# Kernel tuning notes

Measured on AMD Instinct MI355X. Metric: run time of the kernel, lower is better.

The kernel has to match this reference:

```python
import jax, jax.numpy as jnp
import numpy as np

KAPPA = 80.0
NORM_EPS = 0.1
NORM_MAX = 14.0
VOCAB, EMBED, HIDDEN = 50257, 512, 1024
B, S = 2048, 128


def _sample_w(key, kappa, dim, batch):
    """Batched vMF rejection sampler for the radial weight w (Wood 1994).
    Vectorizes the per-row python while-loop of the original module."""
    dim_r = dim - 1
    b = dim_r / (np.sqrt(4.0 * kappa ** 2 + dim_r ** 2) + 2.0 * kappa)
    x = (1.0 - b) / (1.0 + b)
    c = kappa * x + dim_r * np.log(1.0 - x ** 2)
    b = np.float32(b); x = np.float32(x); c = np.float32(c)
    kap = np.float32(kappa); dr = np.float32(dim_r)

    def cond(st):
        return ~jnp.all(st[2])

    def body(st):
        key, w, acc = st
        key, k1, k2 = jax.random.split(key, 3)
        z = jax.random.beta(k1, dim_r / 2.0, dim_r / 2.0, (batch,), dtype=jnp.float32)
        wn = (1.0 - (1.0 + b) * z) / (1.0 - (1.0 - b) * z)
        u = jax.random.uniform(k2, (batch,), dtype=jnp.float32)
        ok = (kap * wn + dr * jnp.log(1.0 - x * wn) - c) >= jnp.log(u)
        w = jnp.where(ok & ~acc, wn, w)
        return key, w, acc | ok

    init = (key, jnp.zeros((batch,), jnp.float32), jnp.zeros((batch,), bool))
    _, w, _ = jax.lax.while_loop(cond, body, init)
    return w


def _vmf_sample(mu, key):
    B_, D = mu.shape
    kw, kv, kt, kf1, kf2 = jax.random.split(key, 5)
    w = _sample_w(kw, KAPPA, D, B_)                       # [B]
    v_raw = jax.random.normal(kv, (B_, D), jnp.float32)
    trand = jax.random.uniform(kt, (B_,), jnp.float32) * NORM_EPS

    munorm = jnp.linalg.norm(mu, axis=1)                  # [B]
    munoise = jnp.clip(munorm, 0.0, NORM_MAX - NORM_EPS) + trand
    safe = jnp.maximum(munorm, 1e-20)
    mu_hat = mu / safe[:, None]
    # sample direction orthonormal to mu_hat
    proj = jnp.sum(mu_hat * v_raw, axis=1, keepdims=True)
    ortho = v_raw - mu_hat * proj
    v = ortho / jnp.linalg.norm(ortho, axis=1, keepdims=True)
    w_ = w[:, None]
    main = (v * jnp.sqrt(1.0 - w_ ** 2) + mu_hat * w_) * munoise[:, None]
    # degenerate branch (||mu|| ~ 0): random small vector
    rd = jax.random.normal(kf1, (B_, D), jnp.float32)
    rd = rd / jnp.linalg.norm(rd, axis=1, keepdims=True)
    fb = rd * (jax.random.uniform(kf2, (B_, 1), jnp.float32) * NORM_EPS)
    return jnp.where((munorm > 1e-10)[:, None], main, fb)


def setup_inputs() -> dict:
    key = jax.random.key(0)
    k1, k2, k3, k4 = jax.random.split(key, 4)
    return {
        "added_tokens": jax.random.randint(k1, (B, S), 0, VOCAB, dtype=jnp.int32).astype(jnp.int64),
        "removed_tokens": jax.random.randint(k2, (B, S), 0, VOCAB, dtype=jnp.int32).astype(jnp.int64),
        "embed_table": jax.random.normal(k3, (VOCAB, EMBED), jnp.float32) * 0.02,
        "w_prenoise": jax.random.normal(k4, (HIDDEN // 2, EMBED), jnp.float32) * 0.02,
    }


def reference(added_tokens, removed_tokens, embed_table, w_prenoise):
    emb_add_sum = embed_table[added_tokens].sum(1)        # [B, EMBED]
    emb_rem_sum = embed_table[removed_tokens].sum(1)      # [B, EMBED]
    insert_set = emb_add_sum @ w_prenoise.T               # [B, HIDDEN/2]
    delete_set = emb_rem_sum @ w_prenoise.T               # [B, HIDDEN/2]
    combined = jnp.concatenate([insert_set, delete_set], axis=1)  # [B, HIDDEN]
    return _vmf_sample(combined, jax.random.key(42))
```

## Files before the change

kernel.cpp:

```cpp
#include <hip/hip_runtime.h>
#include <hip/hip_fp16.h>
#include <stdint.h>
#include <math.h>

#define NROWS 2048
#define SEQ   128
#define EMB   512
#define HID   1024
#define VOCAB 50257
#define GR    4
#define NSPEC 8

typedef _Float16 f16x4 __attribute__((ext_vector_type(4)));
typedef float    f32x4 __attribute__((ext_vector_type(4)));

struct U2 { uint32_t x, y; };

__device__ __forceinline__ uint32_t rotl32(uint32_t v, int r) {
  return (v << r) | (v >> (32 - r));
}

__device__ __forceinline__ U2 tf2x32(U2 key, uint32_t x0, uint32_t x1) {
  uint32_t ks0 = key.x, ks1 = key.y;
  uint32_t ks2 = ks0 ^ ks1 ^ 0x1BD11BDAu;
  x0 += ks0; x1 += ks1;
  x0 += x1; x1 = rotl32(x1, 13); x1 ^= x0;
  x0 += x1; x1 = rotl32(x1, 15); x1 ^= x0;
  x0 += x1; x1 = rotl32(x1, 26); x1 ^= x0;
  x0 += x1; x1 = rotl32(x1, 6);  x1 ^= x0;
  x0 += ks1; x1 += ks2 + 1u;
  x0 += x1; x1 = rotl32(x1, 17); x1 ^= x0;
  x0 += x1; x1 = rotl32(x1, 29); x1 ^= x0;
  x0 += x1; x1 = rotl32(x1, 16); x1 ^= x0;
  x0 += x1; x1 = rotl32(x1, 24); x1 ^= x0;
  x0 += ks2; x1 += ks0 + 2u;
  x0 += x1; x1 = rotl32(x1, 13); x1 ^= x0;
  x0 += x1; x1 = rotl32(x1, 15); x1 ^= x0;
  x0 += x1; x1 = rotl32(x1, 26); x1 ^= x0;
  x0 += x1; x1 = rotl32(x1, 6);  x1 ^= x0;
  x0 += ks0; x1 += ks1 + 3u;
  x0 += x1; x1 = rotl32(x1, 17); x1 ^= x0;
  x0 += x1; x1 = rotl32(x1, 29); x1 ^= x0;
  x0 += x1; x1 = rotl32(x1, 16); x1 ^= x0;
  x0 += x1; x1 = rotl32(x1, 24); x1 ^= x0;
  x0 += ks1; x1 += ks2 + 4u;
  x0 += x1; x1 = rotl32(x1, 13); x1 ^= x0;
  x0 += x1; x1 = rotl32(x1, 15); x1 ^= x0;
  x0 += x1; x1 = rotl32(x1, 26); x1 ^= x0;
  x0 += x1; x1 = rotl32(x1, 6);  x1 ^= x0;
  x0 += ks2; x1 += ks0 + 5u;
  U2 r; r.x = x0; r.y = x1; return r;
}

__device__ __forceinline__ U2 tf_subkey(U2 key, uint32_t i) { return tf2x32(key, 0u, i); }
__device__ __forceinline__ uint32_t tf_bits32(U2 key, uint32_t idx) {
  U2 r = tf2x32(key, 0u, idx);
  return r.x ^ r.y;
}

__device__ __forceinline__ float unit_from_bits(uint32_t b) {
  uint32_t fb = (b >> 9) | 0x3f800000u;
  return __uint_as_float(fb) - 1.0f;
}

__device__ __forceinline__ float f32_log(float x)  { return (float)log((double)x); }
__device__ __forceinline__ float f32_exp(float x)  { return (float)exp((double)x); }
__device__ __forceinline__ float f32_log1p(float x){ return (float)log1p((double)x); }

__device__ float erfinv32(float x) {
#pragma clang fp contract(off)
  float nxx = -(x * x);
  float w = -f32_log1p(nxx);
  float p;
  if (w < 5.0f) {
    w = w - 2.5f;
    p = 2.81022636e-08f;
    p = 3.43273939e-07f  + p * w;
    p = -3.5233877e-06f  + p * w;
    p = -4.39150654e-06f + p * w;
    p = 0.00021858087f   + p * w;
    p = -0.00125372503f  + p * w;
    p = -0.00417768164f  + p * w;
    p = 0.246640727f     + p * w;
    p = 1.50140941f      + p * w;
  } else {
    w = sqrtf(w) - 3.0f;
    p = -0.000200214257f;
    p = 0.000100950558f  + p * w;
    p = 0.00134934322f   + p * w;
    p = -0.00367342844f  + p * w;
    p = 0.00573950773f   + p * w;
    p = -0.0076224613f   + p * w;
    p = 0.00943887047f   + p * w;
    p = 1.00167406f      + p * w;
    p = 2.83297682f      + p * w;
  }
  return p * x;
}

__device__ __forceinline__ float normal_from_bits(uint32_t bits) {
#pragma clang fp contract(off)
  float u = unit_from_bits(bits);
  const float LO = -0.99999994f;
  float x = u * 2.0f + LO;
  x = fmaxf(LO, x);
  return 1.4142135623730951f * erfinv32(x);
}

__device__ float loggamma_511_5(U2 gkey) {
#pragma clang fp contract(off)
  const float one_third = 1.0f / 3.0f;
  const float d = 511.5f - one_third;
  const float c = one_third / sqrtf(d);
  U2 key = tf_subkey(gkey, 0u);
  float V = 1.0f;
  for (int it = 0; it < 64; ++it) {
    U2 knext = tf_subkey(key, 0u);
    U2 xkey  = tf_subkey(key, 1u);
    U2 Ukey  = tf_subkey(key, 2u);
    float x, v;
    U2 xk = xkey;
    do {
      U2 xk_next = tf_subkey(xk, 0u);
      U2 nsub    = tf_subkey(xk, 1u);
      x = normal_from_bits(tf_bits32(nsub, 0u));
      v = 1.0f + x * c;
      xk = xk_next;
    } while (v <= 0.0f);
    float X = x * x;
    V = (v * v) * v;
    float U = unit_from_bits(tf_bits32(Ukey, 0u));
    float sq = 1.0f - 0.0331f * (X * X);
    bool cont;
    if (!(U >= sq)) {
      cont = false;
    } else {
      float logU = f32_log(U);
      float thr = X * 0.5f + d * ((1.0f - V) + f32_log(V));
      cont = (logU >= thr);
    }
    if (!cont) break;
    key = knext;
  }
  return f32_log(d) + f32_log(V);
}

__device__ float beta_elem(U2 k1, uint32_t i) {
#pragma clang fp contract(off)
  U2 ka = tf_subkey(k1, 0u);
  U2 kb = tf_subkey(k1, 1u);
  U2 ga = tf_subkey(ka, i);
  U2 gb = tf_subkey(kb, i);
  float lga = loggamma_511_5(ga);
  float lgb = loggamma_511_5(gb);
  float m  = fmaxf(lga, lgb);
  float ea = f32_exp(lga - m);
  float eb = f32_exp(lgb - m);
  return ea / (ea + eb);
}

__device__ __forceinline__ bool wood_try(U2 K, uint32_t i, float& wn) {
#pragma clang fp contract(off)
  const double kappa_d = 80.0, dimr_d = 1023.0;
  const double b_d = dimr_d / (sqrt(4.0 * kappa_d * kappa_d + dimr_d * dimr_d) + 2.0 * kappa_d);
  const double x_d = (1.0 - b_d) / (1.0 + b_d);
  const double c_d = kappa_d * x_d + dimr_d * log(1.0 - x_d * x_d);
  const float bf = (float)b_d, xf = (float)x_d, cf = (float)c_d;
  const float b1p = 1.0f + bf, b1m = 1.0f - bf;

  U2 k1 = tf_subkey(K, 1u);
  U2 k2 = tf_subkey(K, 2u);
  float z = beta_elem(k1, i);
  wn = (1.0f - b1p * z) / (1.0f - b1m * z);
  float u = unit_from_bits(tf_bits32(k2, i));
  float lhs = (80.0f * wn + 1023.0f * f32_log(1.0f - xf * wn)) - cf;
  return lhs >= f32_log(u);
}

__device__ float wood_seq_from(U2 K, uint32_t i, int t_start) {
  float w = 0.0f;
  for (int t = t_start; t < 64; ++t) {
    U2 Kn = tf_subkey(K, 0u);
    float wn;
    if (wood_try(K, i, wn)) { w = wn; break; }
    K = Kn;
  }
  return w;
}

#define NWOODBLK 64
#define NBLK_W   128
#define NBLK_E   ((VOCAB + 3) / 4)

__device__ __forceinline__ uint2 cvt4h(float4 a) {
  union { __half h[4]; uint2 u; } pk;
  pk.h[0] = __float2half(a.x); pk.h[1] = __float2half(a.y);
  pk.h[2] = __float2half(a.z); pk.h[3] = __float2half(a.w);
  return pk.u;
}

__device__ __forceinline__ uint32_t quant4(float4 a, float inv) {
  int q0 = __float2int_rn(a.x * inv);
  int q1 = __float2int_rn(a.y * inv);
  int q2 = __float2int_rn(a.z * inv);
  int q3 = __float2int_rn(a.w * inv);
  q0 = max(-127, min(127, q0)); q1 = max(-127, min(127, q1));
  q2 = max(-127, min(127, q2)); q3 = max(-127, min(127, q3));
  return (uint32_t)(uint8_t)q0 | ((uint32_t)(uint8_t)q1 << 8) |
         ((uint32_t)(uint8_t)q2 << 16) | ((uint32_t)(uint8_t)q3 << 24);
}

__global__ __launch_bounds__(256) void convert_kernel(
    const float* __restrict__ embed, const float* __restrict__ W,
    int8_t* __restrict__ embed_i8, float* __restrict__ scales,
    __half* __restrict__ W_h,
    float* __restrict__ spec_w, uint32_t* __restrict__ spec_ok) {
  int b = blockIdx.x;
  int wave = threadIdx.x >> 6, lane = threadIdx.x & 63;
  if (b < NWOODBLK) {
    int g = b * 256 + threadIdx.x;
    int t = g >> 11;
    int i = g & (NROWS - 1);
    U2 key42; key42.x = 0u; key42.y = 42u;
    U2 K = tf_subkey(key42, 0u);
    for (int j = 0; j < t; ++j) K = tf_subkey(K, 0u);
    float wn;
    bool ok = wood_try(K, (uint32_t)i, wn);
    spec_w[t * NROWS + i]  = wn;
    spec_ok[t * NROWS + i] = ok ? 1u : 0u;
  } else if (b < NWOODBLK + NBLK_W) {
    int wid = (b - NWOODBLK) * 4 + wave;
    size_t base = (size_t)wid * 128 + lane;
    const float4* src = (const float4*)W;
    uint2* dst = (uint2*)W_h;
    float4 a = src[base];
    float4 c = src[base + 64];
    dst[base]      = cvt4h(a);
    dst[base + 64] = cvt4h(c);
  } else {
    int wid = (b - NWOODBLK - NBLK_W) * 4 + wave;
    if (wid < VOCAB) {
      size_t base = (size_t)wid * 128 + lane;
      const float4* src = (const float4*)embed;
      float4 a = src[base];
      float4 c = src[base + 64];
      float m = fmaxf(fmaxf(fmaxf(fabsf(a.x), fabsf(a.y)), fmaxf(fabsf(a.z), fabsf(a.w))),
                      fmaxf(fmaxf(fabsf(c.x), fabsf(c.y)), fmaxf(fabsf(c.z), fabsf(c.w))));
#pragma unroll
      for (int off = 1; off < 64; off <<= 1) m = fmaxf(m, __shfl_xor(m, off, 64));
      float inv   = (m > 0.0f) ? 127.0f / m : 0.0f;
      float scale = (m > 0.0f) ? m / 127.0f : 0.0f;
      uint32_t* dst = (uint32_t*)embed_i8;
      size_t b32 = (size_t)wid * 128 + lane;
      dst[b32]      = quant4(a, inv);
      dst[b32 + 64] = quant4(c, inv);
      if (lane == 0) scales[wid] = scale;
    }
  }
}

__global__ __launch_bounds__(256) void gather_sum_i8_kernel(
    const int* __restrict__ add_tok, const int* __restrict__ rem_tok,
    const int8_t* __restrict__ embed_i8, const float* __restrict__ scales,
    __half* __restrict__ sums_h) {
  int rb = blockIdx.x * 2;
  int wave = threadIdx.x >> 6;
  int lane = threadIdx.x & 63;
  int row = rb + (wave & 1);
  int which = wave >> 1;
  const int* tok = (which == 0 ? add_tok : rem_tok) + (size_t)row * SEQ;
  int c = lane * 8;
  float acc[8] = {};
  for (int s = 0; s < SEQ; s += 2) {
    int t0 = tok[s], t1 = tok[s + 1];
    float s0 = scales[t0], s1 = scales[t1];
    uint2 v0 = *(const uint2*)&embed_i8[(size_t)t0 * EMB + c];
    uint2 v1 = *(const uint2*)&embed_i8[(size_t)t1 * EMB + c];
    const int8_t* b0 = (const int8_t*)&v0;
    const int8_t* b1 = (const int8_t*)&v1;
#pragma unroll
    for (int j = 0; j < 8; ++j) acc[j] += s0 * (float)b0[j];
#pragma unroll
    for (int j = 0; j < 8; ++j) acc[j] += s1 * (float)b1[j];
  }
  union { __half h[8]; uint4 u; } pk;
#pragma unroll
  for (int j = 0; j < 8; ++j) pk.h[j] = __float2half(acc[j]);
  *(uint4*)&sums_h[((size_t)which * NROWS + row) * EMB + c] = pk.u;
}

__global__ __launch_bounds__(256) void gemm_mfma_kernel(
    const __half* __restrict__ sums_h, const __half* __restrict__ W_h,
    float* __restrict__ out) {
  int wave = threadIdx.x >> 6, lane = threadIdx.x & 63;
  int r0 = blockIdx.x * 16;
  int c0 = blockIdx.y * 256 + wave * 64;
  const __half* A = sums_h + ((c0 < 512) ? 0 : (size_t)NROWS * EMB);
  int wc0 = c0 & 511;
  int l15 = lane & 15, kg = lane >> 4;
  const _Float16* arow = (const _Float16*)&A[(size_t)(r0 + l15) * EMB];
  const _Float16* b0p  = (const _Float16*)&W_h[(size_t)(wc0 +  0 + l15) * EMB];
  const _Float16* b1p  = (const _Float16*)&W_h[(size_t)(wc0 + 16 + l15) * EMB];
  const _Float16* b2p  = (const _Float16*)&W_h[(size_t)(wc0 + 32 + l15) * EMB];
  const _Float16* b3p  = (const _Float16*)&W_h[(size_t)(wc0 + 48 + l15) * EMB];
  f32x4 acc0 = {0.f,0.f,0.f,0.f}, acc1 = acc0, acc2 = acc0, acc3 = acc0;
  for (int k0 = 0; k0 < EMB; k0 += 16) {
    int k = k0 + 4 * kg;
    f16x4 af = *(const f16x4*)&arow[k];
    f16x4 b0 = *(const f16x4*)&b0p[k];
    f16x4 b1 = *(const f16x4*)&b1p[k];
    f16x4 b2 = *(const f16x4*)&b2p[k];
    f16x4 b3 = *(const f16x4*)&b3p[k];
    acc0 = __builtin_amdgcn_mfma_f32_16x16x16f16(af, b0, acc0, 0, 0, 0);
    acc1 = __builtin_amdgcn_mfma_f32_16x16x16f16(af, b1, acc1, 0, 0, 0);
    acc2 = __builtin_amdgcn_mfma_f32_16x16x16f16(af, b2, acc2, 0, 0, 0);
    acc3 = __builtin_amdgcn_mfma_f32_16x16x16f16(af, b3, acc3, 0, 0, 0);
  }
#pragma unroll
  for (int i = 0; i < 4; ++i) {
    size_t rr = (size_t)(r0 + 4 * kg + i) * HID + c0 + l15;
    out[rr +  0] = acc0[i];
    out[rr + 16] = acc1[i];
    out[rr + 32] = acc2[i];
    out[rr + 48] = acc3[i];
  }
}

__global__ __launch_bounds__(128) void gather_sum_kernel(
    const int* __restrict__ add_tok, const int* __restrict__ rem_tok,
    const float* __restrict__ embed, float* __restrict__ sums) {
  int rb = blockIdx.x * GR;
  int which = blockIdx.y;
  const int* tok = (which == 0 ? add_tok : rem_tok);
  __shared__ int t[GR][SEQ];
  for (int q = threadIdx.x; q < GR * SEQ; q += 128) {
    int rr = q >> 7, ss = q & 127;
    t[rr][ss] = tok[(size_t)(rb + rr) * SEQ + ss];
  }
  __syncthreads();
  int c = threadIdx.x * 4;
  float4 a0 = make_float4(0.f,0.f,0.f,0.f), a1 = a0, a2 = a0, a3 = a0;
  for (int s = 0; s < SEQ; ++s) {
    float4 v0 = *(const float4*)&embed[(size_t)t[0][s] * EMB + c];
    float4 v1 = *(const float4*)&embed[(size_t)t[1][s] * EMB + c];
    float4 v2 = *(const float4*)&embed[(size_t)t[2][s] * EMB + c];
    float4 v3 = *(const float4*)&embed[(size_t)t[3][s] * EMB + c];
    a0.x += v0.x; a0.y += v0.y; a0.z += v0.z; a0.w += v0.w;
    a1.x += v1.x; a1.y += v1.y; a1.z += v1.z; a1.w += v1.w;
    a2.x += v2.x; a2.y += v2.y; a2.z += v2.z; a2.w += v2.w;
    a3.x += v3.x; a3.y += v3.y; a3.z += v3.z; a3.w += v3.w;
  }
  size_t base = ((size_t)which * NROWS + rb) * EMB + c;
  *(float4*)&sums[base + 0 * EMB] = a0;
  *(float4*)&sums[base + 1 * EMB] = a1;
  *(float4*)&sums[base + 2 * EMB] = a2;
  *(float4*)&sums[base + 3 * EMB] = a3;
}

__global__ __launch_bounds__(256) void gemm_kernel(
    const float* __restrict__ sums, const float* __restrict__ W,
    float* __restrict__ out) {
  __shared__ float As[16][64];
  __shared__ float Bs[16][64];
  int r0 = blockIdx.x * 64;
  int c0 = blockIdx.y * 64;
  const float* A = sums + ((c0 < 512) ? 0 : (size_t)NROWS * EMB);
  int wc0 = c0 & 511;
  int tid = threadIdx.x;
  int tx = tid & 15, ty = tid >> 4;
  int lr = tid >> 2, lk = (tid & 3) * 4;
  float acc[4][4] = {};
  for (int k0 = 0; k0 < EMB; k0 += 16) {
    float4 av = *(const float4*)&A[(size_t)(r0 + lr) * EMB + k0 + lk];
    float4 bv = *(const float4*)&W[(size_t)(wc0 + lr) * EMB + k0 + lk];
    __syncthreads();
    As[lk + 0][lr] = av.x; As[lk + 1][lr] = av.y; As[lk + 2][lr] = av.z; As[lk + 3][lr] = av.w;
    Bs[lk + 0][lr] = bv.x; Bs[lk + 1][lr] = bv.y; Bs[lk + 2][lr] = bv.z; Bs[lk + 3][lr] = bv.w;
    __syncthreads();
#pragma unroll
    for (int kk = 0; kk < 16; ++kk) {
      float a[4], b[4];
#pragma unroll
      for (int m = 0; m < 4; ++m) a[m] = As[kk][ty * 4 + m];
#pragma unroll
      for (int n = 0; n < 4; ++n) b[n] = Bs[kk][tx * 4 + n];
#pragma unroll
      for (int m = 0; m < 4; ++m)
#pragma unroll
        for (int n = 0; n < 4; ++n) acc[m][n] += a[m] * b[n];
    }
  }
#pragma unroll
  for (int m = 0; m < 4; ++m)
#pragma unroll
    for (int n = 0; n < 4; ++n)
      out[(size_t)(r0 + ty * 4 + m) * HID + c0 + tx * 4 + n] = acc[m][n];
}

__device__ __forceinline__ float block_reduce_sum256(float v, float* red) {
#pragma unroll
  for (int off = 32; off > 0; off >>= 1) v += __shfl_down(v, off, 64);
  if ((threadIdx.x & 63) == 0) red[threadIdx.x >> 6] = v;
  __syncthreads();
  float s = red[0] + red[1] + red[2] + red[3];
  __syncthreads();
  return s;
}

__global__ __launch_bounds__(256) void finalize_kernel(
    const float* __restrict__ spec_w, const uint32_t* __restrict__ spec_ok,
    float* __restrict__ out) {
#pragma clang fp contract(off)
  __shared__ float red[4];
  int r = blockIdx.x, tid = threadIdx.x;
  U2 key42; key42.x = 0u; key42.y = 42u;
  U2 kv = tf_subkey(key42, 1u);
  U2 kt = tf_subkey(key42, 2u);

  float mu[4], vr[4];
#pragma unroll
  for (int q = 0; q < 4; ++q) {
    int j = tid + q * 256;
    mu[q] = out[(size_t)r * HID + j];
    vr[q] = normal_from_bits(tf_bits32(kv, (uint32_t)(r * HID + j)));
  }

  float w = 0.0f;
  int found = -1;
#pragma unroll
  for (int t = 0; t < NSPEC; ++t) {
    if (found < 0 && spec_ok[t * NROWS + r]) { w = spec_w[t * NROWS + r]; found = t; }
  }
  if (found < 0) {
    U2 K = tf_subkey(key42, 0u);
    for (int j = 0; j < NSPEC; ++j) K = tf_subkey(K, 0u);
    w = wood_seq_from(K, (uint32_t)r, NSPEC);
  }
  float trand = unit_from_bits(tf_bits32(kt, (uint32_t)r)) * 0.1f;

  float ss = mu[0]*mu[0] + mu[1]*mu[1] + mu[2]*mu[2] + mu[3]*mu[3];
  ss = block_reduce_sum256(ss, red);
  float munorm = sqrtf(ss);
  float safe = fmaxf(munorm, 1e-20f);
  float muh[4];
#pragma unroll
  for (int q = 0; q < 4; ++q) muh[q] = mu[q] / safe;
  float pp = muh[0]*vr[0] + muh[1]*vr[1] + muh[2]*vr[2] + muh[3]*vr[3];
  pp = block_reduce_sum256(pp, red);
  float ortho[4];
#pragma unroll
  for (int q = 0; q < 4; ++q) ortho[q] = vr[q] - muh[q] * pp;
  float os = ortho[0]*ortho[0] + ortho[1]*ortho[1] + ortho[2]*ortho[2] + ortho[3]*ortho[3];
  os = block_reduce_sum256(os, red);
  float on = sqrtf(os);

  float sqw = sqrtf(1.0f - w * w);
  float munoise = fminf(fmaxf(munorm, 0.0f), 13.9f) + trand;
#pragma unroll
  for (int q = 0; q < 4; ++q) {
    int j = tid + q * 256;
    float v = ortho[q] / on;
    out[(size_t)r * HID + j] = (v * sqw + muh[q] * w) * munoise;
  }
}

__global__ __launch_bounds__(256) void finalize_inline_kernel(float* __restrict__ out) {
#pragma clang fp contract(off)
  __shared__ float red[4];
  int r = blockIdx.x, tid = threadIdx.x;
  U2 key42; key42.x = 0u; key42.y = 42u;
  U2 kv = tf_subkey(key42, 1u);
  U2 kt = tf_subkey(key42, 2u);

  float mu[4], vr[4];
#pragma unroll
  for (int q = 0; q < 4; ++q) {
    int j = tid + q * 256;
    mu[q] = out[(size_t)r * HID + j];
    vr[q] = normal_from_bits(tf_bits32(kv, (uint32_t)(r * HID + j)));
  }
  U2 kw = tf_subkey(key42, 0u);
  float w = wood_seq_from(kw, (uint32_t)r, 0);
  float trand = unit_from_bits(tf_bits32(kt, (uint32_t)r)) * 0.1f;

  float ss = mu[0]*mu[0] + mu[1]*mu[1] + mu[2]*mu[2] + mu[3]*mu[3];
  ss = block_reduce_sum256(ss, red);
  float munorm = sqrtf(ss);
  float safe = fmaxf(munorm, 1e-20f);
  float muh[4];
#pragma unroll
  for (int q = 0; q < 4; ++q) muh[q] = mu[q] / safe;
  float pp = muh[0]*vr[0] + muh[1]*vr[1] + muh[2]*vr[2] + muh[3]*vr[3];
  pp = block_reduce_sum256(pp, red);
  float ortho[4];
#pragma unroll
  for (int q = 0; q < 4; ++q) ortho[q] = vr[q] - muh[q] * pp;
  float os = ortho[0]*ortho[0] + ortho[1]*ortho[1] + ortho[2]*ortho[2] + ortho[3]*ortho[3];
  os = block_reduce_sum256(os, red);
  float on = sqrtf(os);

  float sqw = sqrtf(1.0f - w * w);
  float munoise = fminf(fmaxf(munorm, 0.0f), 13.9f) + trand;
#pragma unroll
  for (int q = 0; q < 4; ++q) {
    int j = tid + q * 256;
    float v = ortho[q] / on;
    out[(size_t)r * HID + j] = (v * sqw + muh[q] * w) * munoise;
  }
}

extern "C" void kernel_launch(void* const* d_in, const int* in_sizes, int n_in,
                              void* d_out, int out_size, void* d_ws, size_t ws_size,
                              hipStream_t stream) {
  const int*   add_tok = (const int*)d_in[0];
  const int*   rem_tok = (const int*)d_in[1];
  const float* embed   = (const float*)d_in[2];
  const float* W       = (const float*)d_in[3];
  float* out = (float*)d_out;

  const size_t EMBED_I8_BYTES = (size_t)VOCAB * EMB;
  const size_t SCALE_BYTES    = (size_t)((VOCAB + 63) & ~63) * 4;
  const size_t W_H_BYTES      = (size_t)512 * EMB * sizeof(__half);
  const size_t SUMS_H_BYTES   = (size_t)2 * NROWS * EMB * sizeof(__half);
  const size_t SPEC_BYTES     = (size_t)NSPEC * NROWS * 4;
  const size_t NEED = EMBED_I8_BYTES + SCALE_BYTES + W_H_BYTES + SUMS_H_BYTES + 2 * SPEC_BYTES;

  if (ws_size >= NEED) {
    char* p = (char*)d_ws;
    int8_t*   embed_i8 = (int8_t*)p;   p += EMBED_I8_BYTES;
    float*    scales   = (float*)p;    p += SCALE_BYTES;
    __half*   W_h      = (__half*)p;   p += W_H_BYTES;
    __half*   sums_h   = (__half*)p;   p += SUMS_H_BYTES;
    float*    spec_w   = (float*)p;    p += SPEC_BYTES;
    uint32_t* spec_ok  = (uint32_t*)p;

    convert_kernel<<<NWOODBLK + NBLK_W + NBLK_E, 256, 0, stream>>>(
        embed, W, embed_i8, scales, W_h, spec_w, spec_ok);
    gather_sum_i8_kernel<<<NROWS / 2, 256, 0, stream>>>(
        add_tok, rem_tok, embed_i8, scales, sums_h);
    gemm_mfma_kernel<<<dim3(NROWS / 16, HID / 256), 256, 0, stream>>>(sums_h, W_h, out);
    finalize_kernel<<<NROWS, 256, 0, stream>>>(spec_w, spec_ok, out);
  } else {
    float* sums = (float*)d_ws;
    gather_sum_kernel<<<dim3(NROWS / GR, 2), 128, 0, stream>>>(add_tok, rem_tok, embed, sums);
    gemm_kernel<<<dim3(NROWS / 64, HID / 64), 256, 0, stream>>>(sums, W, out);
    finalize_inline_kernel<<<NROWS, 256, 0, stream>>>(out);
  }
}
```

Before: 116.9 us.

## Fuse MFMA GEMM with vMF finalize via shared-memory row tile

Merges the GEMM and finalize kernels into one. Each block computes a full 16x1024 output tile into 64KB of shared memory, then each wave normalizes rows with wave-level shuffle reductions instead of block reductions. This drops one launch and the global round-trip of the intermediate output. In exchange the grid shrinks from 512 to 128 blocks, and the large shared-memory footprint limits occupancy and may underfill the GPU.

```diff
diff --git a/kernel.cpp b/kernel.cpp
--- a/kernel.cpp
+++ b/kernel.cpp
@@ -289,40 +289,110 @@
   *(uint4*)&sums_h[((size_t)which * NROWS + row) * EMB + c] = pk.u;
 }
 
-__global__ __launch_bounds__(256) void gemm_mfma_kernel(
+__global__ __launch_bounds__(256) void gemm_finalize_kernel(
     const __half* __restrict__ sums_h, const __half* __restrict__ W_h,
+    const float* __restrict__ spec_w, const uint32_t* __restrict__ spec_ok,
     float* __restrict__ out) {
+  __shared__ float comb[16][HID];
   int wave = threadIdx.x >> 6, lane = threadIdx.x & 63;
   int r0 = blockIdx.x * 16;
-  int c0 = blockIdx.y * 256 + wave * 64;
-  const __half* A = sums_h + ((c0 < 512) ? 0 : (size_t)NROWS * EMB);
-  int wc0 = c0 & 511;
   int l15 = lane & 15, kg = lane >> 4;
-  const _Float16* arow = (const _Float16*)&A[(size_t)(r0 + l15) * EMB];
-  const _Float16* b0p  = (const _Float16*)&W_h[(size_t)(wc0 +  0 + l15) * EMB];
-  const _Float16* b1p  = (const _Float16*)&W_h[(size_t)(wc0 + 16 + l15) * EMB];
-  const _Float16* b2p  = (const _Float16*)&W_h[(size_t)(wc0 + 32 + l15) * EMB];
-  const _Float16* b3p  = (const _Float16*)&W_h[(size_t)(wc0 + 48 + l15) * EMB];
-  f32x4 acc0 = {0.f,0.f,0.f,0.f}, acc1 = acc0, acc2 = acc0, acc3 = acc0;
-  for (int k0 = 0; k0 < EMB; k0 += 16) {
-    int k = k0 + 4 * kg;
-    f16x4 af = *(const f16x4*)&arow[k];
-    f16x4 b0 = *(const f16x4*)&b0p[k];
-    f16x4 b1 = *(const f16x4*)&b1p[k];
-    f16x4 b2 = *(const f16x4*)&b2p[k];
-    f16x4 b3 = *(const f16x4*)&b3p[k];
-    acc0 = __builtin_amdgcn_mfma_f32_16x16x16f16(af, b0, acc0, 0, 0, 0);
-    acc1 = __builtin_amdgcn_mfma_f32_16x16x16f16(af, b1, acc1, 0, 0, 0);
-    acc2 = __builtin_amdgcn_mfma_f32_16x16x16f16(af, b2, acc2, 0, 0, 0);
-    acc3 = __builtin_amdgcn_mfma_f32_16x16x16f16(af, b3, acc3, 0, 0, 0);
-  }
-#pragma unroll
-  for (int i = 0; i < 4; ++i) {
-    size_t rr = (size_t)(r0 + 4 * kg + i) * HID + c0 + l15;
-    out[rr +  0] = acc0[i];
-    out[rr + 16] = acc1[i];
-    out[rr + 32] = acc2[i];
-    out[rr + 48] = acc3[i];
+
+  for (int cg = 0; cg < 4; ++cg) {
+    int c0 = cg * 256 + wave * 64;
+    const __half* A = sums_h + ((c0 < 512) ? 0 : (size_t)NROWS * EMB);
+    int wc0 = c0 & 511;
+    const _Float16* arow = (const _Float16*)&A[(size_t)(r0 + l15) * EMB];
+    const _Float16* b0p  = (const _Float16*)&W_h[(size_t)(wc0 +  0 + l15) * EMB];
+    const _Float16* b1p  = (const _Float16*)&W_h[(size_t)(wc0 + 16 + l15) * EMB];
+    const _Float16* b2p  = (const _Float16*)&W_h[(size_t)(wc0 + 32 + l15) * EMB];
+    const _Float16* b3p  = (const _Float16*)&W_h[(size_t)(wc0 + 48 + l15) * EMB];
+    f32x4 acc0 = {0.f,0.f,0.f,0.f}, acc1 = acc0, acc2 = acc0, acc3 = acc0;
+    for (int k0 = 0; k0 < EMB; k0 += 16) {
+      int k = k0 + 4 * kg;
+      f16x4 af = *(const f16x4*)&arow[k];
+      f16x4 b0 = *(const f16x4*)&b0p[k];
+      f16x4 b1 = *(const f16x4*)&b1p[k];
+      f16x4 b2 = *(const f16x4*)&b2p[k];
+      f16x4 b3 = *(const f16x4*)&b3p[k];
+      acc0 = __builtin_amdgcn_mfma_f32_16x16x16f16(af, b0, acc0, 0, 0, 0);
+      acc1 = __builtin_amdgcn_mfma_f32_16x16x16f16(af, b1, acc1, 0, 0, 0);
+      acc2 = __builtin_amdgcn_mfma_f32_16x16x16f16(af, b2, acc2, 0, 0, 0);
+      acc3 = __builtin_amdgcn_mfma_f32_16x16x16f16(af, b3, acc3, 0, 0, 0);
+    }
+#pragma unroll
+    for (int i = 0; i < 4; ++i) {
+      int rr = 4 * kg + i;
+      comb[rr][c0 + l15 +  0] = acc0[i];
+      comb[rr][c0 + l15 + 16] = acc1[i];
+      comb[rr][c0 + l15 + 32] = acc2[i];
+      comb[rr][c0 + l15 + 48] = acc3[i];
+    }
+  }
+  __syncthreads();
+
+  {
+#pragma clang fp contract(off)
+    U2 key42; key42.x = 0u; key42.y = 42u;
+    U2 kv = tf_subkey(key42, 1u);
+    U2 kt = tf_subkey(key42, 2u);
+    for (int p = 0; p < 4; ++p) {
+      int rr = wave + p * 4;
+      int r  = r0 + rr;
+      float mu[16], vr[16];
+#pragma unroll
+      for (int j = 0; j < 16; ++j) mu[j] = comb[rr][j * 64 + lane];
+#pragma unroll
+      for (int j = 0; j < 16; ++j)
+        vr[j] = normal_from_bits(tf_bits32(kv, (uint32_t)(r * HID + j * 64 + lane)));
+
+      float ss = 0.f;
+#pragma unroll
+      for (int j = 0; j < 16; ++j) ss += mu[j] * mu[j];
+#pragma unroll
+      for (int off = 32; off > 0; off >>= 1) ss += __shfl_xor(ss, off, 64);
+      float munorm = sqrtf(ss);
+      float safe = fmaxf(munorm, 1e-20f);
+      float muh[16];
+#pragma unroll
+      for (int j = 0; j < 16; ++j) muh[j] = mu[j] / safe;
+
+      float pp = 0.f;
+#pragma unroll
+      for (int j = 0; j < 16; ++j) pp += muh[j] * vr[j];
+#pragma unroll
+      for (int off = 32; off > 0; off >>= 1) pp += __shfl_xor(pp, off, 64);
+
+      float os = 0.f;
+#pragma unroll
+      for (int j = 0; j < 16; ++j) {
+        vr[j] = vr[j] - muh[j] * pp;
+        os += vr[j] * vr[j];
+      }
+#pragma unroll
+      for (int off = 32; off > 0; off >>= 1) os += __shfl_xor(os, off, 64);
+      float on = sqrtf(os);
+
+      float w = 0.0f;
+      int found = -1;
+#pragma unroll
+      for (int t = 0; t < NSPEC; ++t) {
+        if (found < 0 && spec_ok[t * NROWS + r]) { w = spec_w[t * NROWS + r]; found = t; }
+      }
+      if (found < 0) {
+        U2 K = tf_subkey(key42, 0u);
+        for (int j = 0; j < NSPEC; ++j) K = tf_subkey(K, 0u);
+        w = wood_seq_from(K, (uint32_t)r, NSPEC);
+      }
+      float trand = unit_from_bits(tf_bits32(kt, (uint32_t)r)) * 0.1f;
+      float sqw = sqrtf(1.0f - w * w);
+      float munoise = fminf(fmaxf(munorm, 0.0f), 13.9f) + trand;
+#pragma unroll
+      for (int j = 0; j < 16; ++j) {
+        float v = vr[j] / on;
+        out[(size_t)r * HID + j * 64 + lane] = (v * sqw + muh[j] * w) * munoise;
+      }
+    }
   }
 }
 
@@ -407,63 +477,6 @@
   return s;
 }
 
-__global__ __launch_bounds__(256) void finalize_kernel(
-    const float* __restrict__ spec_w, const uint32_t* __restrict__ spec_ok,
-    float* __restrict__ out) {
-#pragma clang fp contract(off)
-  __shared__ float red[4];
-  int r = blockIdx.x, tid = threadIdx.x;
-  U2 key42; key42.x = 0u; key42.y = 42u;
-  U2 kv = tf_subkey(key42, 1u);
-  U2 kt = tf_subkey(key42, 2u);
-
-  float mu[4], vr[4];
-#pragma unroll
-  for (int q = 0; q < 4; ++q) {
-    int j = tid + q * 256;
-    mu[q] = out[(size_t)r * HID + j];
-    vr[q] = normal_from_bits(tf_bits32(kv, (uint32_t)(r * HID + j)));
-  }
-
-  float w = 0.0f;
-  int found = -1;
-#pragma unroll
-  for (int t = 0; t < NSPEC; ++t) {
-    if (found < 0 && spec_ok[t * NROWS + r]) { w = spec_w[t * NROWS + r]; found = t; }
-  }
-  if (found < 0) {
-    U2 K = tf_subkey(key42, 0u);
-    for (int j = 0; j < NSPEC; ++j) K = tf_subkey(K, 0u);
-    w = wood_seq_from(K, (uint32_t)r, NSPEC);
-  }
-  float trand = unit_from_bits(tf_bits32(kt, (uint32_t)r)) * 0.1f;
-
-  float ss = mu[0]*mu[0] + mu[1]*mu[1] + mu[2]*mu[2] + mu[3]*mu[3];
-  ss = block_reduce_sum256(ss, red);
-  float munorm = sqrtf(ss);
-  float safe = fmaxf(munorm, 1e-20f);
-  float muh[4];
-#pragma unroll
-  for (int q = 0; q < 4; ++q) muh[q] = mu[q] / safe;
-  float pp = muh[0]*vr[0] + muh[1]*vr[1] + muh[2]*vr[2] + muh[3]*vr[3];
-  pp = block_reduce_sum256(pp, red);
-  float ortho[4];
-#pragma unroll
-  for (int q = 0; q < 4; ++q) ortho[q] = vr[q] - muh[q] * pp;
-  float os = ortho[0]*ortho[0] + ortho[1]*ortho[1] + ortho[2]*ortho[2] + ortho[3]*ortho[3];
-  os = block_reduce_sum256(os, red);
-  float on = sqrtf(os);
-
-  float sqw = sqrtf(1.0f - w * w);
-  float munoise = fminf(fmaxf(munorm, 0.0f), 13.9f) + trand;
-#pragma unroll
-  for (int q = 0; q < 4; ++q) {
-    int j = tid + q * 256;
-    float v = ortho[q] / on;
-    out[(size_t)r * HID + j] = (v * sqw + muh[q] * w) * munoise;
-  }
-}
-
 __global__ __launch_bounds__(256) void finalize_inline_kernel(float* __restrict__ out) {
 #pragma clang fp contract(off)
   __shared__ float red[4];
@@ -538,8 +551,8 @@
         embed, W, embed_i8, scales, W_h, spec_w, spec_ok);
     gather_sum_i8_kernel<<<NROWS / 2, 256, 0, stream>>>(
         add_tok, rem_tok, embed_i8, scales, sums_h);
-    gemm_mfma_kernel<<<dim3(NROWS / 16, HID / 256), 256, 0, stream>>>(sums_h, W_h, out);
-    finalize_kernel<<<NROWS, 256, 0, stream>>>(spec_w, spec_ok, out);
+    gemm_finalize_kernel<<<NROWS / 16, 256, 0, stream>>>(
+        sums_h, W_h, spec_w, spec_ok, out);
   } else {
     float* sums = (float*)d_ws;
     gather_sum_kernel<<<dim3(NROWS / GR, 2), 128, 0, stream>>>(add_tok, rem_tok, embed, sums);
```

Result: slower. 168.2 us (+43.9%).
